# Kernel optimization log

Hardware: AMD Instinct MI355X
Metric: run time of the kernel (lower is better)

## Reference

```python
import jax, jax.numpy as jnp
import numpy as np

N = 50000   # nodes
E = 800000  # edges (avg degree 16)
D = 2048    # resnet50 feature dim
C = 256     # layer_size
NEG_SLOPE = 0.2


def setup_inputs() -> dict:
    key = jax.random.key(0)
    ks = jax.random.split(key, 16)
    s = 0.02
    inp = {
        'x': jax.random.normal(ks[0], (N, D), jnp.float32),
        'edge_index': jax.random.randint(ks[1], (2, E), 0, N, dtype=jnp.int32),
        # GATConv layer 1 (in=D, out=C, heads=1)
        'W1': jax.random.normal(ks[2], (D, C), jnp.float32) * s,
        'a_src1': jax.random.normal(ks[3], (C,), jnp.float32) * s,
        'a_dst1': jax.random.normal(ks[4], (C,), jnp.float32) * s,
        'b1': jnp.zeros((C,), jnp.float32),
        # GATConv layer 2 (in=C, out=C)
        'W2': jax.random.normal(ks[5], (C, C), jnp.float32) * s,
        'a_src2': jax.random.normal(ks[6], (C,), jnp.float32) * s,
        'a_dst2': jax.random.normal(ks[7], (C,), jnp.float32) * s,
        'b2': jnp.zeros((C,), jnp.float32),
        # EdgePredictor: lin1 (2C -> C), lin2 (C -> 1)
        'Wp1': jax.random.normal(ks[8], (2 * C, C), jnp.float32) * s,
        'bp1': jnp.zeros((C,), jnp.float32),
        'wp2': jax.random.normal(ks[9], (C,), jnp.float32) * s,
        'bp2': jnp.zeros((), jnp.float32),
    }
    return inp


def gat_layer(x, src, dst, W, a_src, a_dst, b, n_nodes):
    # PyG GATConv, heads=1, concat=True: message flows src -> dst,
    # softmax over incoming edges of each dst node.
    h = x @ W                                   # [N, C]
    e = jax.nn.leaky_relu((h @ a_src)[src] + (h @ a_dst)[dst], NEG_SLOPE)  # [E]
    emax = jax.ops.segment_max(e, dst, num_segments=n_nodes)
    ex = jnp.exp(e - emax[dst])
    denom = jax.ops.segment_sum(ex, dst, num_segments=n_nodes)
    alpha = ex / (denom[dst] + 1e-16)           # [E]
    out = jax.ops.segment_sum(h[src] * alpha[:, None], dst, num_segments=n_nodes)
    return out + b


def reference(x, edge_index, W1, a_src1, a_dst1, b1, W2, a_src2, a_dst2, b2,
              Wp1, bp1, wp2, bp2):
    src, dst = edge_index[0], edge_index[1]
    # GATConv default add_self_loops=True
    loops = jnp.arange(N, dtype=src.dtype)
    src_sl = jnp.concatenate([src, loops])
    dst_sl = jnp.concatenate([dst, loops])

    h = gat_layer(x, src_sl, dst_sl, W1, a_src1, a_dst1, b1, N)
    h = gat_layer(h, src_sl, dst_sl, W2, a_src2, a_dst2, b2, N)

    # edge predictor on the ORIGINAL edge_index (no self loops)
    xe = jnp.concatenate([h[src], h[dst]], axis=-1)       # [E, 2C]
    z = jax.nn.relu(xe @ Wp1 + bp1)                        # [E, C]  (dropout: eval mode)
    return z @ wp2 + bp2                                   # [E]
```

## Files before the change

### kernel.cpp

```cpp
#include <hip/hip_runtime.h>
#include <hip/hip_bf16.h>
#include <stdint.h>

#define NNODES 50000
#define NEDGES 800000
#define DIN    2048
#define CDIM   256
#define ELOOP  (NEDGES + NNODES)

using bf16x8 = __attribute__((ext_vector_type(8))) short;
using f32x4  = __attribute__((ext_vector_type(4))) float;
using gvoid  = __attribute__((address_space(1))) const void;
using lvoid  = __attribute__((address_space(3))) void;

__device__ __forceinline__ float bf2f(uint16_t u) {
    union { uint32_t i; float f; } v; v.i = (uint32_t)u << 16; return v.f;
}
__device__ __forceinline__ uint16_t f2bf(float f) {
    union { float f; uint32_t i; } v; v.f = f;
    uint32_t i = v.i;
    return (uint16_t)((i + 0x7FFFu + ((i >> 16) & 1u)) >> 16);
}

#define BM 128
#define BN 128
#define BK 32

__global__ __launch_bounds__(256)
void gemm_bt(const uint16_t* __restrict__ A, const uint16_t* __restrict__ Bt,
             uint16_t* __restrict__ C, const float* __restrict__ bias,
             int M, int N, int K)
{
    __shared__ __align__(16) uint16_t lA[2][BM * BK];
    __shared__ __align__(16) uint16_t lB[2][BN * BK];
    const int tid  = threadIdx.x;
    const int wave = tid >> 6;
    const int lane = tid & 63;
    const int lm = lane & 15, lq = lane >> 4;
    const int bm = blockIdx.x * BM;
    const int bn = blockIdx.y * BN;
    const int wm = (wave >> 1) * 64;
    const int wn = (wave & 1) * 64;

    f32x4 acc[4][4];
    for (int i = 0; i < 4; ++i)
        for (int j = 0; j < 4; ++j)
            acc[i][j] = (f32x4)0.0f;

    auto stage = [&](int buf, int k0) {
        for (int j = 0; j < 2; ++j) {
            int c = j * 256 + wave * 64 + lane;
            int row = c >> 2, cc = c & 3;
            int gr = bm + row; if (gr >= M) gr = M - 1;
            const uint16_t* gp = A + (size_t)gr * K + k0 + cc * 8;
            __builtin_amdgcn_global_load_lds((gvoid*)gp,
                (lvoid*)(lA[buf] + (size_t)(j * 256 + wave * 64) * 8), 16, 0, 0);
        }
        for (int j = 0; j < 2; ++j) {
            int c = j * 256 + wave * 64 + lane;
            int row = c >> 2, cc = c & 3;
            int gr = bn + row; if (gr >= N) gr = N - 1;
            const uint16_t* gp = Bt + (size_t)gr * K + k0 + cc * 8;
            __builtin_amdgcn_global_load_lds((gvoid*)gp,
                (lvoid*)(lB[buf] + (size_t)(j * 256 + wave * 64) * 8), 16, 0, 0);
        }
    };

    const int nt = K / BK;
    stage(0, 0);
    __syncthreads();
    int cur = 0;
    for (int t = 0; t < nt; ++t) {
        if (t + 1 < nt) stage(cur ^ 1, (t + 1) * BK);

        bf16x8 af[4], bfr[4];
        for (int mt = 0; mt < 4; ++mt)
            af[mt] = *(const bf16x8*)(lA[cur] + (wm + mt * 16 + lm) * BK + lq * 8);
        for (int nt2 = 0; nt2 < 4; ++nt2)
            bfr[nt2] = *(const bf16x8*)(lB[cur] + (wn + nt2 * 16 + lm) * BK + lq * 8);

        for (int mt = 0; mt < 4; ++mt)
            for (int nt2 = 0; nt2 < 4; ++nt2)
                acc[mt][nt2] = __builtin_amdgcn_mfma_f32_16x16x32_bf16(
                    af[mt], bfr[nt2], acc[mt][nt2], 0, 0, 0);
        __syncthreads();
        cur ^= 1;
    }

    for (int mt = 0; mt < 4; ++mt) {
        for (int nt2 = 0; nt2 < 4; ++nt2) {
            int gn = bn + wn + nt2 * 16 + lm;
            float badd = bias ? bias[gn] : 0.0f;
            for (int r = 0; r < 4; ++r) {
                int gm = bm + wm + mt * 16 + lq * 4 + r;
                if (gm < M)
                    C[(size_t)gm * N + gn] = f2bf(acc[mt][nt2][r] + badd);
            }
        }
    }
}

__global__ __launch_bounds__(256)
void gemm_f32_bt(const float* __restrict__ A, const uint16_t* __restrict__ Bt,
                 uint16_t* __restrict__ C, int M, int N, int K)
{
    __shared__ __align__(16) float    lA[2][BM * BK];
    __shared__ __align__(16) uint16_t lB[2][BN * BK];
    const int tid  = threadIdx.x;
    const int wave = tid >> 6;
    const int lane = tid & 63;
    const int lm = lane & 15, lq = lane >> 4;
    const int bm = blockIdx.x * BM;
    const int bn = blockIdx.y * BN;
    const int wm = (wave >> 1) * 64;
    const int wn = (wave & 1) * 64;

    f32x4 acc[4][4];
    for (int i = 0; i < 4; ++i)
        for (int j = 0; j < 4; ++j)
            acc[i][j] = (f32x4)0.0f;

    auto stage = [&](int buf, int k0) {
        for (int j = 0; j < 4; ++j) {
            int c = j * 256 + wave * 64 + lane;
            int row = c >> 3;
            int lc  = (c & 7) ^ (row & 7);
            int gr = bm + row; if (gr >= M) gr = M - 1;
            const float* gp = A + (size_t)gr * K + k0 + lc * 4;
            __builtin_amdgcn_global_load_lds((gvoid*)gp,
                (lvoid*)(lA[buf] + (size_t)(j * 256 + wave * 64) * 4), 16, 0, 0);
        }
        for (int j = 0; j < 2; ++j) {
            int c = j * 256 + wave * 64 + lane;
            int row = c >> 2, cc = c & 3;
            int gr = bn + row; if (gr >= N) gr = N - 1;
            const uint16_t* gp = Bt + (size_t)gr * K + k0 + cc * 8;
            __builtin_amdgcn_global_load_lds((gvoid*)gp,
                (lvoid*)(lB[buf] + (size_t)(j * 256 + wave * 64) * 8), 16, 0, 0);
        }
    };

    const int nt = K / BK;
    stage(0, 0);
    __syncthreads();
    int cur = 0;
    for (int t = 0; t < nt; ++t) {
        if (t + 1 < nt) stage(cur ^ 1, (t + 1) * BK);

        bf16x8 af[4], bfr[4];
        for (int mt = 0; mt < 4; ++mt) {
            int r = wm + mt * 16 + lm;
            int s0 = (lq * 2)     ^ (r & 7);
            int s1 = (lq * 2 + 1) ^ (r & 7);
            f32x4 a0 = *(const f32x4*)(lA[cur] + r * BK + s0 * 4);
            f32x4 a1 = *(const f32x4*)(lA[cur] + r * BK + s1 * 4);
            bf16x8 t2;
            for (int q = 0; q < 4; ++q) {
                t2[q]     = (short)f2bf(a0[q]);
                t2[q + 4] = (short)f2bf(a1[q]);
            }
            af[mt] = t2;
        }
        for (int nt2 = 0; nt2 < 4; ++nt2)
            bfr[nt2] = *(const bf16x8*)(lB[cur] + (wn + nt2 * 16 + lm) * BK + lq * 8);

        for (int mt = 0; mt < 4; ++mt)
            for (int nt2 = 0; nt2 < 4; ++nt2)
                acc[mt][nt2] = __builtin_amdgcn_mfma_f32_16x16x32_bf16(
                    af[mt], bfr[nt2], acc[mt][nt2], 0, 0, 0);
        __syncthreads();
        cur ^= 1;
    }

    for (int mt = 0; mt < 4; ++mt) {
        for (int nt2 = 0; nt2 < 4; ++nt2) {
            int gn = bn + wn + nt2 * 16 + lm;
            for (int r = 0; r < 4; ++r) {
                int gm = bm + wm + mt * 16 + lq * 4 + r;
                if (gm < M)
                    C[(size_t)gm * N + gn] = f2bf(acc[mt][nt2][r]);
            }
        }
    }
}

__global__ void transpose_cvt_kernel(const float* __restrict__ W,
                                     uint16_t* __restrict__ Wt, int K, int N)
{
    int idx = blockIdx.x * 256 + threadIdx.x;
    if (idx >= K * N) return;
    int n = idx / K, k = idx - n * K;
    Wt[idx] = f2bf(W[(size_t)k * N + n]);
}

__global__ void bias512_kernel(const float* __restrict__ bp1,
                               float* __restrict__ bias512)
{
    int i = blockIdx.x * 256 + threadIdx.x;
    if (i < 512) bias512[i] = (i < 256) ? bp1[i] : 0.0f;
}

__global__ void count_kernel(const int* __restrict__ ei, int* __restrict__ rs)
{
    int i = blockIdx.x * 256 + threadIdx.x;
    if (i >= ELOOP) return;
    int dst = (i < NEDGES) ? ei[NEDGES + i] : (i - NEDGES);
    atomicAdd(&rs[dst + 1], 1);
}

__global__ __launch_bounds__(1024)
void scan_kernel(int* __restrict__ rs, int* __restrict__ cursor)
{
    __shared__ int wsum[16];
    const int tid = threadIdx.x, lane = tid & 63, w = tid >> 6;
    int carry = 0;
    for (int base = 0; base <= NNODES; base += 1024) {
        int i = base + tid;
        int v = (i <= NNODES) ? rs[i] : 0;
        int s = v;
        for (int d = 1; d < 64; d <<= 1) {
            int t = __shfl_up(s, d);
            if (lane >= d) s += t;
        }
        if (lane == 63) wsum[w] = s;
        __syncthreads();
        if (tid < 16) {
            int x = wsum[tid];
            for (int d = 1; d < 16; d <<= 1) {
                int t = __shfl_up(x, d);
                if (tid >= d) x += t;
            }
            wsum[tid] = x;
        }
        __syncthreads();
        int incl = s + carry + (w > 0 ? wsum[w - 1] : 0);
        if (i <= NNODES) {
            rs[i] = incl;
            if (i < NNODES) cursor[i] = incl;
        }
        int total = carry + wsum[15];
        __syncthreads();
        carry = total;
    }
}

__global__ void fill_kernel(const int* __restrict__ ei, int* __restrict__ cursor,
                            int* __restrict__ csr_src)
{
    int i = blockIdx.x * 256 + threadIdx.x;
    if (i >= ELOOP) return;
    int src, dst;
    if (i < NEDGES) { src = ei[i]; dst = ei[NEDGES + i]; }
    else            { src = dst = i - NEDGES; }
    int pos = atomicAdd(&cursor[dst], 1);
    csr_src[pos] = src;
}

__global__ __launch_bounds__(256)
void rowdot_kernel(const uint16_t* __restrict__ g,
                   const float* __restrict__ asrc,
                   const float* __restrict__ adst,
                   float* __restrict__ s_src, float* __restrict__ s_dst)
{
    int n = blockIdx.x * 4 + (threadIdx.x >> 6);
    int lane = threadIdx.x & 63;
    ushort4 rv = *(const ushort4*)(g + (size_t)n * CDIM + lane * 4);
    float4 av = *(const float4*)(asrc + lane * 4);
    float4 dv = *(const float4*)(adst + lane * 4);
    float r0 = bf2f(rv.x), r1 = bf2f(rv.y), r2 = bf2f(rv.z), r3 = bf2f(rv.w);
    float a = r0 * av.x + r1 * av.y + r2 * av.z + r3 * av.w;
    float b = r0 * dv.x + r1 * dv.y + r2 * dv.z + r3 * dv.w;
    for (int d = 32; d; d >>= 1) { a += __shfl_xor(a, d); b += __shfl_xor(b, d); }
    if (lane == 0) { s_src[n] = a; s_dst[n] = b; }
}

__global__ __launch_bounds__(256)
void attn_kernel(const int* __restrict__ row_start, const int* __restrict__ csr_src,
                 const float* __restrict__ s_src, const float* __restrict__ s_dst,
                 const uint16_t* __restrict__ g, const float* __restrict__ bvec,
                 uint16_t* __restrict__ hout)
{
    int n = blockIdx.x * 4 + (threadIdx.x >> 6);
    int lane = threadIdx.x & 63;
    int beg = row_start[n], end = row_start[n + 1];
    float sdn = s_dst[n];

    float m = -1e30f;
    for (int i = beg + lane; i < end; i += 64) {
        float e = s_src[csr_src[i]] + sdn;
        e = (e > 0.f) ? e : 0.2f * e;
        m = fmaxf(m, e);
    }
    for (int d = 32; d; d >>= 1) m = fmaxf(m, __shfl_xor(m, d));

    float sum = 0.f;
    for (int i = beg + lane; i < end; i += 64) {
        float e = s_src[csr_src[i]] + sdn;
        e = (e > 0.f) ? e : 0.2f * e;
        sum += __expf(e - m);
    }
    for (int d = 32; d; d >>= 1) sum += __shfl_xor(sum, d);
    float inv = 1.f / (sum + 1e-16f);

    float a0 = 0.f, a1 = 0.f, a2 = 0.f, a3 = 0.f;
    for (int i = beg; i < end; ++i) {
        int src = csr_src[i];
        float e = s_src[src] + sdn;
        e = (e > 0.f) ? e : 0.2f * e;
        float alpha = __expf(e - m) * inv;
        ushort4 rv = *(const ushort4*)(g + (size_t)src * CDIM + lane * 4);
        a0 += alpha * bf2f(rv.x);
        a1 += alpha * bf2f(rv.y);
        a2 += alpha * bf2f(rv.z);
        a3 += alpha * bf2f(rv.w);
    }
    float4 bv = *(const float4*)(bvec + lane * 4);
    ushort4 o;
    o.x = f2bf(a0 + bv.x);
    o.y = f2bf(a1 + bv.y);
    o.z = f2bf(a2 + bv.z);
    o.w = f2bf(a3 + bv.w);
    *(ushort4*)(hout + (size_t)n * CDIM + lane * 4) = o;
}

__global__ __launch_bounds__(256)
void edgepred_kernel(const int* __restrict__ ei,
                     const uint16_t* __restrict__ UV,
                     const float* __restrict__ wp2, const float* __restrict__ bp2,
                     float* __restrict__ out)
{
    const int tid = threadIdx.x;
    const int grp = tid >> 4, l = tid & 15;
    const int e = blockIdx.x * 16 + grp;
    int src = ei[e];
    int dst = ei[NEDGES + e];
    const uint16_t* Up = UV + (size_t)src * 512 + l * 16;
    const uint16_t* Vp = UV + (size_t)dst * 512 + 256 + l * 16;
    const uint4 u0 = *(const uint4*)(Up);
    const uint4 u1 = *(const uint4*)(Up + 8);
    const uint4 v0 = *(const uint4*)(Vp);
    const uint4 v1 = *(const uint4*)(Vp + 8);
    const float4 w0 = *(const float4*)(wp2 + l * 16);
    const float4 w1 = *(const float4*)(wp2 + l * 16 + 4);
    const float4 w2 = *(const float4*)(wp2 + l * 16 + 8);
    const float4 w3 = *(const float4*)(wp2 + l * 16 + 12);
    float acc = 0.f;
    auto proc = [&](uint32_t uu, uint32_t vv, float wa, float wb) {
        float z0 = fmaxf(bf2f((uint16_t)(uu & 0xffffu)) + bf2f((uint16_t)(vv & 0xffffu)), 0.f);
        float z1 = fmaxf(bf2f((uint16_t)(uu >> 16)) + bf2f((uint16_t)(vv >> 16)), 0.f);
        acc += z0 * wa + z1 * wb;
    };
    proc(u0.x, v0.x, w0.x, w0.y); proc(u0.y, v0.y, w0.z, w0.w);
    proc(u0.z, v0.z, w1.x, w1.y); proc(u0.w, v0.w, w1.z, w1.w);
    proc(u1.x, v1.x, w2.x, w2.y); proc(u1.y, v1.y, w2.z, w2.w);
    proc(u1.z, v1.z, w3.x, w3.y); proc(u1.w, v1.w, w3.z, w3.w);
    for (int d = 1; d < 16; d <<= 1) acc += __shfl_xor(acc, d);
    if (l == 0) out[e] = acc + *bp2;
}

extern "C" void kernel_launch(void* const* d_in, const int* in_sizes, int n_in,
                              void* d_out, int out_size, void* d_ws, size_t ws_size,
                              hipStream_t stream)
{
    const float* x   = (const float*)d_in[0];
    const int*   ei  = (const int*)d_in[1];
    const float* W1  = (const float*)d_in[2];
    const float* as1 = (const float*)d_in[3];
    const float* ad1 = (const float*)d_in[4];
    const float* b1  = (const float*)d_in[5];
    const float* W2  = (const float*)d_in[6];
    const float* as2 = (const float*)d_in[7];
    const float* ad2 = (const float*)d_in[8];
    const float* b2  = (const float*)d_in[9];
    const float* Wp1 = (const float*)d_in[10];
    const float* bp1 = (const float*)d_in[11];
    const float* wp2 = (const float*)d_in[12];
    const float* bp2 = (const float*)d_in[13];
    float* out = (float*)d_out;

    char* ws = (char*)d_ws;
    size_t off = 0;
    auto alloc = [&](size_t bytes) -> void* {
        void* p = ws + off;
        off += (bytes + 255) & ~(size_t)255;
        return p;
    };
    uint16_t* W1t   = (uint16_t*)alloc((size_t)DIN * CDIM * 2);
    uint16_t* W2t   = (uint16_t*)alloc((size_t)CDIM * CDIM * 2);
    uint16_t* WpABt = (uint16_t*)alloc((size_t)2 * CDIM * CDIM * 2);
    int* row_start = (int*)alloc((NNODES + 1) * sizeof(int));
    int* cursor    = (int*)alloc(NNODES * sizeof(int));
    int* csr_src   = (int*)alloc((size_t)ELOOP * sizeof(int));
    float* s_src   = (float*)alloc(NNODES * sizeof(float));
    float* s_dst   = (float*)alloc(NNODES * sizeof(float));
    float* bias512 = (float*)alloc(512 * sizeof(float));
    uint16_t* H    = (uint16_t*)alloc((size_t)NNODES * CDIM * 2);
    uint16_t* G    = (uint16_t*)alloc((size_t)NNODES * CDIM * 2);
    uint16_t* Vb   = (uint16_t*)alloc((size_t)NNODES * CDIM * 2);
    uint16_t* UV   = G;

    hipMemsetAsync(row_start, 0, (NNODES + 1) * sizeof(int), stream);

    transpose_cvt_kernel<<<(DIN * CDIM + 255) / 256, 256, 0, stream>>>(W1, W1t, DIN, CDIM);
    transpose_cvt_kernel<<<(CDIM * CDIM + 255) / 256, 256, 0, stream>>>(W2, W2t, CDIM, CDIM);
    transpose_cvt_kernel<<<(CDIM * CDIM + 255) / 256, 256, 0, stream>>>(Wp1, WpABt, CDIM, CDIM);
    transpose_cvt_kernel<<<(CDIM * CDIM + 255) / 256, 256, 0, stream>>>(Wp1 + CDIM * CDIM, WpABt + CDIM * CDIM, CDIM, CDIM);
    bias512_kernel<<<2, 256, 0, stream>>>(bp1, bias512);

    count_kernel<<<(ELOOP + 255) / 256, 256, 0, stream>>>(ei, row_start);
    scan_kernel<<<1, 1024, 0, stream>>>(row_start, cursor);
    fill_kernel<<<(ELOOP + 255) / 256, 256, 0, stream>>>(ei, cursor, csr_src);

    dim3 gg((NNODES + BM - 1) / BM, CDIM / BN);

    gemm_f32_bt<<<gg, 256, 0, stream>>>(x, W1t, G, NNODES, CDIM, DIN);
    rowdot_kernel<<<NNODES / 4, 256, 0, stream>>>(G, as1, ad1, s_src, s_dst);
    attn_kernel<<<NNODES / 4, 256, 0, stream>>>(row_start, csr_src, s_src, s_dst, G, b1, H);

    gemm_bt<<<gg, 256, 0, stream>>>(H, W2t, G, nullptr, NNODES, CDIM, CDIM);
    rowdot_kernel<<<NNODES / 4, 256, 0, stream>>>(G, as2, ad2, s_src, s_dst);
    attn_kernel<<<NNODES / 4, 256, 0, stream>>>(row_start, csr_src, s_src, s_dst, G, b2, H);

    dim3 gg2((NNODES + BM - 1) / BM, 512 / BN);
    gemm_bt<<<gg2, 256, 0, stream>>>(H, WpABt, UV, bias512, NNODES, 512, CDIM);

    edgepred_kernel<<<NEDGES / 16, 256, 0, stream>>>(ei, UV, wp2, bp2, out);
}
```

Baseline: 1.239 ms.

## Triple-buffer GEMM loads, tile weight transpose, parallelize scan, widen attention gathers

Both GEMM kernels move from double to triple-buffered LDS staging. Prefetch runs two tiles ahead, gated by explicit vmcnt waits and raw barriers in place of __syncthreads. The weight transpose now goes through a 32x33 shared tile, and the single-block CSR scan becomes a three-kernel multi-block scan. The attention aggregation has each half-wave take alternate edges with 16-byte loads, then combines the halves with a cross-lane shuffle. Together these aim to hide global-load latency, cut serial scan time and raise gather bandwidth, at the cost of more LDS per block (possibly lower occupancy) and hand-tuned waitcnt values that must match the number of outstanding loads.

```diff
diff --git a/kernel.cpp b/kernel.cpp
--- a/kernel.cpp
+++ b/kernel.cpp
@@ -26,13 +26,15 @@
 #define BN 128
 #define BK 32
 
+#define WAITVM(N) asm volatile("s_waitcnt vmcnt(" #N ")" ::: "memory")
+
 __global__ __launch_bounds__(256)
 void gemm_bt(const uint16_t* __restrict__ A, const uint16_t* __restrict__ Bt,
              uint16_t* __restrict__ C, const float* __restrict__ bias,
              int M, int N, int K)
 {
-    __shared__ __align__(16) uint16_t lA[2][BM * BK];
-    __shared__ __align__(16) uint16_t lB[2][BN * BK];
+    __shared__ __align__(16) uint16_t lA[3][BM * BK];
+    __shared__ __align__(16) uint16_t lB[3][BN * BK];
     const int tid  = threadIdx.x;
     const int wave = tid >> 6;
     const int lane = tid & 63;
@@ -59,19 +61,21 @@
         for (int j = 0; j < 2; ++j) {
             int c = j * 256 + wave * 64 + lane;
             int row = c >> 2, cc = c & 3;
-            int gr = bn + row; if (gr >= N) gr = N - 1;
-            const uint16_t* gp = Bt + (size_t)gr * K + k0 + cc * 8;
+            const uint16_t* gp = Bt + (size_t)(bn + row) * K + k0 + cc * 8;
             __builtin_amdgcn_global_load_lds((gvoid*)gp,
                 (lvoid*)(lB[buf] + (size_t)(j * 256 + wave * 64) * 8), 16, 0, 0);
         }
     };
 
-    const int nt = K / BK;
+    const int ntiles = K / BK;
     stage(0, 0);
-    __syncthreads();
-    int cur = 0;
-    for (int t = 0; t < nt; ++t) {
-        if (t + 1 < nt) stage(cur ^ 1, (t + 1) * BK);
+    stage(1, BK);
+    WAITVM(4);
+    __builtin_amdgcn_s_barrier();
+
+    for (int t = 0; t < ntiles; ++t) {
+        const int cur = t % 3;
+        if (t + 2 < ntiles) stage((t + 2) % 3, (t + 2) * BK);
 
         bf16x8 af[4], bfr[4];
         for (int mt = 0; mt < 4; ++mt)
@@ -83,8 +87,12 @@
             for (int nt2 = 0; nt2 < 4; ++nt2)
                 acc[mt][nt2] = __builtin_amdgcn_mfma_f32_16x16x32_bf16(
                     af[mt], bfr[nt2], acc[mt][nt2], 0, 0, 0);
-        __syncthreads();
-        cur ^= 1;
+
+        if (t + 1 < ntiles) {
+            if (t + 2 < ntiles) WAITVM(4);
+            else                WAITVM(0);
+            __builtin_amdgcn_s_barrier();
+        }
     }
 
     for (int mt = 0; mt < 4; ++mt) {
@@ -104,8 +112,8 @@
 void gemm_f32_bt(const float* __restrict__ A, const uint16_t* __restrict__ Bt,
                  uint16_t* __restrict__ C, int M, int N, int K)
 {
-    __shared__ __align__(16) float    lA[2][BM * BK];
-    __shared__ __align__(16) uint16_t lB[2][BN * BK];
+    __shared__ __align__(16) float    lA[3][BM * BK];
+    __shared__ __align__(16) uint16_t lB[3][BN * BK];
     const int tid  = threadIdx.x;
     const int wave = tid >> 6;
     const int lane = tid & 63;
@@ -133,19 +141,21 @@
         for (int j = 0; j < 2; ++j) {
             int c = j * 256 + wave * 64 + lane;
             int row = c >> 2, cc = c & 3;
-            int gr = bn + row; if (gr >= N) gr = N - 1;
-            const uint16_t* gp = Bt + (size_t)gr * K + k0 + cc * 8;
+            const uint16_t* gp = Bt + (size_t)(bn + row) * K + k0 + cc * 8;
             __builtin_amdgcn_global_load_lds((gvoid*)gp,
                 (lvoid*)(lB[buf] + (size_t)(j * 256 + wave * 64) * 8), 16, 0, 0);
         }
     };
 
-    const int nt = K / BK;
+    const int ntiles = K / BK;
     stage(0, 0);
-    __syncthreads();
-    int cur = 0;
-    for (int t = 0; t < nt; ++t) {
-        if (t + 1 < nt) stage(cur ^ 1, (t + 1) * BK);
+    stage(1, BK);
+    WAITVM(6);
+    __builtin_amdgcn_s_barrier();
+
+    for (int t = 0; t < ntiles; ++t) {
+        const int cur = t % 3;
+        if (t + 2 < ntiles) stage((t + 2) % 3, (t + 2) * BK);
 
         bf16x8 af[4], bfr[4];
         for (int mt = 0; mt < 4; ++mt) {
@@ -168,8 +178,12 @@
             for (int nt2 = 0; nt2 < 4; ++nt2)
                 acc[mt][nt2] = __builtin_amdgcn_mfma_f32_16x16x32_bf16(
                     af[mt], bfr[nt2], acc[mt][nt2], 0, 0, 0);
-        __syncthreads();
-        cur ^= 1;
+
+        if (t + 1 < ntiles) {
+            if (t + 2 < ntiles) WAITVM(6);
+            else                WAITVM(0);
+            __builtin_amdgcn_s_barrier();
+        }
     }
 
     for (int mt = 0; mt < 4; ++mt) {
@@ -184,13 +198,18 @@
     }
 }
 
-__global__ void transpose_cvt_kernel(const float* __restrict__ W,
-                                     uint16_t* __restrict__ Wt, int K, int N)
-{
-    int idx = blockIdx.x * 256 + threadIdx.x;
-    if (idx >= K * N) return;
-    int n = idx / K, k = idx - n * K;
-    Wt[idx] = f2bf(W[(size_t)k * N + n]);
+__global__ __launch_bounds__(256)
+void transpose_cvt_kernel(const float* __restrict__ W,
+                          uint16_t* __restrict__ Wt, int K, int N)
+{
+    __shared__ float tile[32][33];
+    const int k0 = blockIdx.x * 32, n0 = blockIdx.y * 32;
+    const int tx = threadIdx.x & 31, ty = threadIdx.x >> 5;
+    for (int r = 0; r < 32; r += 8)
+        tile[ty + r][tx] = W[(size_t)(k0 + ty + r) * N + n0 + tx];
+    __syncthreads();
+    for (int r = 0; r < 32; r += 8)
+        Wt[(size_t)(n0 + ty + r) * K + k0 + tx] = f2bf(tile[tx][ty + r]);
 }
 
 __global__ void bias512_kernel(const float* __restrict__ bp1,
@@ -209,38 +228,55 @@
 }
 
 __global__ __launch_bounds__(1024)
-void scan_kernel(int* __restrict__ rs, int* __restrict__ cursor)
+void scan_part_kernel(int* __restrict__ rs, int* __restrict__ bsum)
 {
     __shared__ int wsum[16];
-    const int tid = threadIdx.x, lane = tid & 63, w = tid >> 6;
-    int carry = 0;
-    for (int base = 0; base <= NNODES; base += 1024) {
-        int i = base + tid;
-        int v = (i <= NNODES) ? rs[i] : 0;
-        int s = v;
-        for (int d = 1; d < 64; d <<= 1) {
-            int t = __shfl_up(s, d);
-            if (lane >= d) s += t;
-        }
-        if (lane == 63) wsum[w] = s;
-        __syncthreads();
-        if (tid < 16) {
-            int x = wsum[tid];
-            for (int d = 1; d < 16; d <<= 1) {
-                int t = __shfl_up(x, d);
-                if (tid >= d) x += t;
-            }
-            wsum[tid] = x;
-        }
-        __syncthreads();
-        int incl = s + carry + (w > 0 ? wsum[w - 1] : 0);
-        if (i <= NNODES) {
-            rs[i] = incl;
-            if (i < NNODES) cursor[i] = incl;
-        }
-        int total = carry + wsum[15];
-        __syncthreads();
-        carry = total;
+    const int b = blockIdx.x, tid = threadIdx.x, lane = tid & 63, w = tid >> 6;
+    int i = b * 1024 + tid;
+    int v = (i <= NNODES) ? rs[i] : 0;
+    int s = v;
+    for (int d = 1; d < 64; d <<= 1) {
+        int t = __shfl_up(s, d);
+        if (lane >= d) s += t;
+    }
+    if (lane == 63) wsum[w] = s;
+    __syncthreads();
+    if (tid < 16) {
+        int x = wsum[tid];
+        for (int d = 1; d < 16; d <<= 1) {
+            int t = __shfl_up(x, d);
+            if (tid >= d) x += t;
+        }
+        wsum[tid] = x;
+    }
+    __syncthreads();
+    int incl = s + (w > 0 ? wsum[w - 1] : 0);
+    if (i <= NNODES) rs[i] = incl;
+    if (tid == 1023) bsum[b] = incl;
+}
+
+__global__ void scan_bsum_kernel(int* __restrict__ bsum, int nb)
+{
+    int tid = threadIdx.x;
+    int v = (tid < nb) ? bsum[tid] : 0;
+    for (int d = 1; d < 64; d <<= 1) {
+        int t = __shfl_up(v, d);
+        if (tid >= d) v += t;
+    }
+    if (tid < nb) bsum[tid] = v;
+}
+
+__global__ __launch_bounds__(1024)
+void scan_add_kernel(const int* __restrict__ bsum, int* __restrict__ rs,
+                     int* __restrict__ cursor)
+{
+    int b = blockIdx.x;
+    int i = b * 1024 + threadIdx.x;
+    int add = b ? bsum[b - 1] : 0;
+    if (i <= NNODES) {
+        int r = rs[i] + add;
+        rs[i] = r;
+        if (i < NNODES) cursor[i] = r;
     }
 }
 
@@ -282,6 +318,7 @@
 {
     int n = blockIdx.x * 4 + (threadIdx.x >> 6);
     int lane = threadIdx.x & 63;
+    int h = lane >> 5, hl = lane & 31;
     int beg = row_start[n], end = row_start[n + 1];
     float sdn = s_dst[n];
 
@@ -303,24 +340,37 @@
     float inv = 1.f / (sum + 1e-16f);
 
     float a0 = 0.f, a1 = 0.f, a2 = 0.f, a3 = 0.f;
-    for (int i = beg; i < end; ++i) {
+    float a4 = 0.f, a5 = 0.f, a6 = 0.f, a7 = 0.f;
+    for (int i = beg + h; i < end; i += 2) {
         int src = csr_src[i];
         float e = s_src[src] + sdn;
         e = (e > 0.f) ? e : 0.2f * e;
         float alpha = __expf(e - m) * inv;
-        ushort4 rv = *(const ushort4*)(g + (size_t)src * CDIM + lane * 4);
-        a0 += alpha * bf2f(rv.x);
-        a1 += alpha * bf2f(rv.y);
-        a2 += alpha * bf2f(rv.z);
-        a3 += alpha * bf2f(rv.w);
-    }
-    float4 bv = *(const float4*)(bvec + lane * 4);
-    ushort4 o;
-    o.x = f2bf(a0 + bv.x);
-    o.y = f2bf(a1 + bv.y);
-    o.z = f2bf(a2 + bv.z);
-    o.w = f2bf(a3 + bv.w);
-    *(ushort4*)(hout + (size_t)n * CDIM + lane * 4) = o;
+        uint4 rv = *(const uint4*)(g + (size_t)src * CDIM + hl * 8);
+        a0 += alpha * bf2f((uint16_t)(rv.x & 0xffffu));
+        a1 += alpha * bf2f((uint16_t)(rv.x >> 16));
+        a2 += alpha * bf2f((uint16_t)(rv.y & 0xffffu));
+        a3 += alpha * bf2f((uint16_t)(rv.y >> 16));
+        a4 += alpha * bf2f((uint16_t)(rv.z & 0xffffu));
+        a5 += alpha * bf2f((uint16_t)(rv.z >> 16));
+        a6 += alpha * bf2f((uint16_t)(rv.w & 0xffffu));
+        a7 += alpha * bf2f((uint16_t)(rv.w >> 16));
+    }
+    a0 += __shfl_xor(a0, 32); a1 += __shfl_xor(a1, 32);
+    a2 += __shfl_xor(a2, 32); a3 += __shfl_xor(a3, 32);
+    a4 += __shfl_xor(a4, 32); a5 += __shfl_xor(a5, 32);
+    a6 += __shfl_xor(a6, 32); a7 += __shfl_xor(a7, 32);
+
+    if (h == 0) {
+        const float4 b0 = *(const float4*)(bvec + hl * 8);
+        const float4 b1 = *(const float4*)(bvec + hl * 8 + 4);
+        uint4 o;
+        o.x = (uint32_t)f2bf(a0 + b0.x) | ((uint32_t)f2bf(a1 + b0.y) << 16);
+        o.y = (uint32_t)f2bf(a2 + b0.z) | ((uint32_t)f2bf(a3 + b0.w) << 16);
+        o.z = (uint32_t)f2bf(a4 + b1.x) | ((uint32_t)f2bf(a5 + b1.y) << 16);
+        o.w = (uint32_t)f2bf(a6 + b1.z) | ((uint32_t)f2bf(a7 + b1.w) << 16);
+        *(uint4*)(hout + (size_t)n * CDIM + hl * 8) = o;
+    }
 }
 
 __global__ __launch_bounds__(256)
@@ -391,24 +441,29 @@
     int* row_start = (int*)alloc((NNODES + 1) * sizeof(int));
     int* cursor    = (int*)alloc(NNODES * sizeof(int));
     int* csr_src   = (int*)alloc((size_t)ELOOP * sizeof(int));
+    int* bsum      = (int*)alloc(64 * sizeof(int));
     float* s_src   = (float*)alloc(NNODES * sizeof(float));
     float* s_dst   = (float*)alloc(NNODES * sizeof(float));
     float* bias512 = (float*)alloc(512 * sizeof(float));
     uint16_t* H    = (uint16_t*)alloc((size_t)NNODES * CDIM * 2);
     uint16_t* G    = (uint16_t*)alloc((size_t)NNODES * CDIM * 2);
     uint16_t* Vb   = (uint16_t*)alloc((size_t)NNODES * CDIM * 2);
+    (void)Vb;
     uint16_t* UV   = G;
 
     hipMemsetAsync(row_start, 0, (NNODES + 1) * sizeof(int), stream);
 
-    transpose_cvt_kernel<<<(DIN * CDIM + 255) / 256, 256, 0, stream>>>(W1, W1t, DIN, CDIM);
-    transpose_cvt_kernel<<<(CDIM * CDIM + 255) / 256, 256, 0, stream>>>(W2, W2t, CDIM, CDIM);
-    transpose_cvt_kernel<<<(CDIM * CDIM + 255) / 256, 256, 0, stream>>>(Wp1, WpABt, CDIM, CDIM);
-    transpose_cvt_kernel<<<(CDIM * CDIM + 255) / 256, 256, 0, stream>>>(Wp1 + CDIM * CDIM, WpABt + CDIM * CDIM, CDIM, CDIM);
+    transpose_cvt_kernel<<<dim3(DIN / 32, CDIM / 32), 256, 0, stream>>>(W1, W1t, DIN, CDIM);
+    transpose_cvt_kernel<<<dim3(CDIM / 32, CDIM / 32), 256, 0, stream>>>(W2, W2t, CDIM, CDIM);
+    transpose_cvt_kernel<<<dim3(CDIM / 32, CDIM / 32), 256, 0, stream>>>(Wp1, WpABt, CDIM, CDIM);
+    transpose_cvt_kernel<<<dim3(CDIM / 32, CDIM / 32), 256, 0, stream>>>(Wp1 + CDIM * CDIM, WpABt + CDIM * CDIM, CDIM, CDIM);
     bias512_kernel<<<2, 256, 0, stream>>>(bp1, bias512);
 
+    const int NB = (NNODES + 1 + 1023) / 1024;
     count_kernel<<<(ELOOP + 255) / 256, 256, 0, stream>>>(ei, row_start);
-    scan_kernel<<<1, 1024, 0, stream>>>(row_start, cursor);
+    scan_part_kernel<<<NB, 1024, 0, stream>>>(row_start, bsum);
+    scan_bsum_kernel<<<1, 64, 0, stream>>>(bsum, NB);
+    scan_add_kernel<<<NB, 1024, 0, stream>>>(bsum, row_start, cursor);
     fill_kernel<<<(ELOOP + 255) / 256, 256, 0, stream>>>(ei, cursor, csr_src);
 
     dim3 gg((NNODES + BM - 1) / BM, CDIM / BN);
```

Measured after the change: 1.146 ms. -7.5%, faster.
